# Kernel tuning notes

Hardware: AMD Instinct MI355X
Metric: run time of the kernel (lower is better)

Reference implementation:

```python
import jax, jax.numpy as jnp
from jax import lax
import numpy as np

EPS_LN = 1e-5
EPS_BN = 1e-5


def _forward(x, prior, alpha, in_proj_w, conv_w, conv_b, x_proj_weight,
             dt_projs_weight, dt_projs_bias, A_logs, Ds, out_norm_w, out_norm_b,
             out_proj_w, p2w_w1, p2w_b1, p2w_bn_w, p2w_bn_b, p2w_bn_mean,
             p2w_bn_var, p2w_w2, p2w_b2):
    Din = conv_w.shape[0]
    # in_proj (Linear2d == 1x1 conv), split into ssm branch and gate z
    xz = jnp.einsum('bchw,dc->bdhw', x, in_proj_w)          # [B, 2*Din, H, W]
    x_ssm, z = jnp.split(xz, 2, axis=1)
    # depthwise 3x3 conv + SiLU
    x_ssm = lax.conv_general_dilated(
        x_ssm, conv_w, (1, 1), 'SAME',
        dimension_numbers=('NCHW', 'OIHW', 'NCHW'),
        feature_group_count=Din) + conv_b[None, :, None, None]
    x_ssm = jax.nn.silu(x_ssm)

    B, D, H, W = x_ssm.shape
    L = H * W
    K = 4
    R = dt_projs_weight.shape[2]
    N = A_logs.shape[1]

    # cross_scan: 4 directions = row-major, col-major, and their reverses
    row = x_ssm.reshape(B, D, L)
    col = x_ssm.transpose(0, 1, 3, 2).reshape(B, D, L)
    xs = jnp.stack([row, col, row[..., ::-1], col[..., ::-1]], axis=1)  # [B,K,D,L]

    x_dbl = jnp.einsum('bkdl,kcd->bkcl', xs, x_proj_weight)  # [B,K,R+2N,L]
    dts, Bs, Cs = jnp.split(x_dbl, [R, R + N], axis=2)       # [B,K,R,L],[B,K,N,L],[B,K,N,L]
    dts = jnp.einsum('bkrl,kdr->bkdl', dts, dt_projs_weight)  # [B,K,D,L]

    A = -jnp.exp(A_logs.astype(jnp.float32)).reshape(K, D, N)
    dt = jax.nn.softplus(dts + dt_projs_bias[None, :, :, None])  # [B,K,D,L]

    dA = jnp.exp(dt[..., None] * A[None, :, :, None, :])          # [B,K,D,L,N]
    dBx = dt[..., None] * Bs.transpose(0, 1, 3, 2)[:, :, None, :, :] * xs[..., None]
    Cseq = Cs.transpose(0, 1, 3, 2)                               # [B,K,L,N]

    dA_t = jnp.moveaxis(dA, 3, 0)    # [L,B,K,D,N]
    dBx_t = jnp.moveaxis(dBx, 3, 0)  # [L,B,K,D,N]
    C_t = jnp.moveaxis(Cseq, 2, 0)   # [L,B,K,N]

    def step(h, inp):
        a, bx, c = inp
        h = h * a + bx                              # [B,K,D,N]
        y = jnp.einsum('bkdn,bkn->bkd', h, c)
        return h, y

    h0 = jnp.zeros((B, K, D, N), dtype=jnp.float32)
    _, ys = lax.scan(step, h0, (dA_t, dBx_t, C_t))  # [L,B,K,D]
    ys = jnp.moveaxis(ys, 0, 3)                     # [B,K,D,L]
    ys = ys + Ds.reshape(K, D)[None, :, :, None] * xs
    ys = ys.reshape(B, K, D, H, W)

    # prior -> per-direction guidance weights (PriorToWeights, BN in eval mode)
    g = jnp.einsum('bchw,oc->bohw', prior, p2w_w1) + p2w_b1[None, :, None, None]
    g = (g - p2w_bn_mean[None, :, None, None]) * jax.lax.rsqrt(
        p2w_bn_var[None, :, None, None] + EPS_BN)
    g = g * p2w_bn_w[None, :, None, None] + p2w_bn_b[None, :, None, None]
    g = jax.nn.relu(g)
    g = jnp.einsum('bchw,oc->bohw', g, p2w_w2) + p2w_b2[None, :, None, None]
    gw = jax.nn.sigmoid(g)                          # [B,4,H,W]
    s = jax.nn.sigmoid(alpha)                       # [1]
    Wdir = 1.0 + s * (gw - 1.0)                     # torch.lerp(ones, gw, s)
    ys = ys * Wdir[:, :, None, :, :]

    # cross_merge: inverse of cross_scan, sum of 4 directions
    ysl = ys.reshape(B, K, D, L)
    y = ysl[:, 0] + ysl[:, 2, :, ::-1]
    yt = ysl[:, 1] + ysl[:, 3, :, ::-1]
    y = y + yt.reshape(B, D, W, H).transpose(0, 1, 3, 2).reshape(B, D, L)
    y = y.reshape(B, D, H, W)

    # LayerNorm2d: normalize over channel dim
    mu = y.mean(axis=1, keepdims=True)
    var = y.var(axis=1, keepdims=True)
    y = (y - mu) * jax.lax.rsqrt(var + EPS_LN)
    y = y * out_norm_w[None, :, None, None] + out_norm_b[None, :, None, None]

    y = y * jax.nn.silu(z)
    out = jnp.einsum('bdhw,md->bmhw', y, out_proj_w)  # out_proj 1x1, no bias
    return out


def setup_inputs() -> dict:
    key = jax.random.key(0)
    ks = jax.random.split(key, 16)
    B, Dm, H, W = 8, 96, 64, 64
    Din, N, K, R, hid = 192, 1, 4, 6, 32

    def rn(k, shape, scale):
        return jax.random.normal(k, shape, jnp.float32) * scale

    return {
        'x': rn(ks[0], (B, Dm, H, W), 1.0),
        'prior': jax.random.uniform(ks[1], (B, 4, H, W), jnp.float32),
        'alpha': rn(ks[2], (1,), 1.0),
        'in_proj_w': rn(ks[3], (2 * Din, Dm), Dm ** -0.5),
        'conv_w': rn(ks[4], (Din, 1, 3, 3), 1.0 / 3.0),
        'conv_b': rn(ks[5], (Din,), 0.1),
        'x_proj_weight': rn(ks[6], (K, R + 2 * N, Din), Din ** -0.5),
        'dt_projs_weight': rn(ks[7], (K, Din, R), R ** -0.5),
        'dt_projs_bias': rn(ks[8], (K, Din), 0.5) - 4.0,
        'A_logs': jnp.tile(jnp.log(jnp.arange(1, N + 1, dtype=jnp.float32)), (K * Din, 1)),
        'Ds': jnp.ones((K * Din,), jnp.float32),
        'out_norm_w': jnp.ones((Din,), jnp.float32),
        'out_norm_b': jnp.zeros((Din,), jnp.float32),
        'out_proj_w': rn(ks[9], (Dm, Din), Din ** -0.5),
        'p2w_w1': rn(ks[10], (hid, 4), 0.5),
        'p2w_b1': jnp.zeros((hid,), jnp.float32),
        'p2w_bn_w': jnp.ones((hid,), jnp.float32),
        'p2w_bn_b': jnp.zeros((hid,), jnp.float32),
        'p2w_bn_mean': jnp.zeros((hid,), jnp.float32),
        'p2w_bn_var': jnp.ones((hid,), jnp.float32),
        'p2w_w2': rn(ks[11], (4, hid), hid ** -0.5),
        'p2w_b2': jnp.zeros((4,), jnp.float32),
    }


def reference(x, prior, alpha, in_proj_w, conv_w, conv_b, x_proj_weight,
              dt_projs_weight, dt_projs_bias, A_logs, Ds, out_norm_w, out_norm_b,
              out_proj_w, p2w_w1, p2w_b1, p2w_bn_w, p2w_bn_b, p2w_bn_mean,
              p2w_bn_var, p2w_w2, p2w_b2):
    return _forward(x, prior, alpha, in_proj_w, conv_w, conv_b, x_proj_weight,
                    dt_projs_weight, dt_projs_bias, A_logs, Ds, out_norm_w,
                    out_norm_b, out_proj_w, p2w_w1, p2w_b1, p2w_bn_w, p2w_bn_b,
                    p2w_bn_mean, p2w_bn_var, p2w_w2, p2w_b2)
```

## Files before the change

kernel.cpp:

```cpp
#include <hip/hip_runtime.h>

#define BB   8
#define CIN  96
#define DIN  192
#define HH   64
#define WW   64
#define LL   4096
#define KK   4
#define COUT 96
#define SS   128
#define LC   32

#define LOG2E 1.4426950408889634f
#define LN2   0.6931471805599453f

typedef unsigned short bf16t;
typedef float f32x2 __attribute__((ext_vector_type(2)));

__device__ __forceinline__ f32x2 pkfma(f32x2 a, f32x2 b, f32x2 c) {
#if __has_builtin(__builtin_elementwise_fma)
  return __builtin_elementwise_fma(a, b, c);
#else
  f32x2 r;
  r[0] = fmaf(a[0], b[0], c[0]);
  r[1] = fmaf(a[1], b[1], c[1]);
  return r;
#endif
}

__device__ __forceinline__ float exp2fast(float x) { return __builtin_amdgcn_exp2f(x); }
__device__ __forceinline__ float log2fast(float x) { return __builtin_amdgcn_logf(x); }
__device__ __forceinline__ float sigf(float x) { return 1.0f / (1.0f + __expf(-x)); }
__device__ __forceinline__ int trp(int p) { return ((p & 63) << 6) | (p >> 6); }
__device__ __forceinline__ int pix_of(int k, int l) {
  if (k == 0) return l;
  if (k == 1) return trp(l);
  if (k == 2) return LL - 1 - l;
  return trp(LL - 1 - l);
}
__device__ __forceinline__ float b2f(bf16t v) {
  return __uint_as_float((unsigned)v << 16);
}
__device__ __forceinline__ bf16t f2b(float f) {
  unsigned u = __float_as_uint(f);
  return (bf16t)((u + 0x7FFFu + ((u >> 16) & 1u)) >> 16);
}

__global__ __launch_bounds__(256) void gemm_in_k(const float* __restrict__ in,
                                                 const float* __restrict__ W,
                                                 bf16t* __restrict__ out) {
  const int tid = threadIdx.x;
  const int b  = blockIdx.z;
  const int o0 = blockIdx.y * 8;
  const int p0 = blockIdx.x * 1024 + tid * 4;
  const float* inb = in + (size_t)b * CIN * LL + p0;
  const float* Wb  = W + (size_t)o0 * CIN;
  f32x2 accL[8], accH[8];
#pragma unroll
  for (int j = 0; j < 8; ++j) { accL[j] = (f32x2){0.f, 0.f}; accH[j] = (f32x2){0.f, 0.f}; }
#pragma unroll 4
  for (int c = 0; c < CIN; c += 4) {
    float4 w[8];
#pragma unroll
    for (int j = 0; j < 8; ++j) w[j] = *(const float4*)&Wb[j * CIN + c];
    float4 xv[4];
#pragma unroll
    for (int t = 0; t < 4; ++t) xv[t] = *(const float4*)&inb[(size_t)(c + t) * LL];
#pragma unroll
    for (int j = 0; j < 8; ++j) {
#pragma unroll
      for (int t = 0; t < 4; ++t) {
        const float ws = t == 0 ? w[j].x : t == 1 ? w[j].y : t == 2 ? w[j].z : w[j].w;
        const f32x2 wv = {ws, ws};
        accL[j] = pkfma((f32x2){xv[t].x, xv[t].y}, wv, accL[j]);
        accH[j] = pkfma((f32x2){xv[t].z, xv[t].w}, wv, accH[j]);
      }
    }
  }
  bf16t* ob = out + (size_t)b * 384 * LL + p0;
#pragma unroll
  for (int j = 0; j < 8; ++j) {
    ushort4 st;
    st.x = f2b(accL[j][0]);
    st.y = f2b(accL[j][1]);
    st.z = f2b(accH[j][0]);
    st.w = f2b(accH[j][1]);
    *(ushort4*)&ob[(size_t)(o0 + j) * LL] = st;
  }
}

__global__ __launch_bounds__(256) void gemm_out_k(const bf16t* __restrict__ in,
                                                  const float* __restrict__ W,
                                                  float* __restrict__ out) {
  const int tid = threadIdx.x;
  const int b  = blockIdx.z;
  const int o0 = blockIdx.y * 4;
  const int p0 = blockIdx.x * 1024 + tid * 4;
  const bf16t* inb = in + (size_t)b * DIN * LL + p0;
  const float* Wb  = W + (size_t)o0 * DIN;
  f32x2 accL[4], accH[4];
#pragma unroll
  for (int j = 0; j < 4; ++j) { accL[j] = (f32x2){0.f, 0.f}; accH[j] = (f32x2){0.f, 0.f}; }
#pragma unroll 4
  for (int c = 0; c < DIN; c += 4) {
    float4 w[4];
#pragma unroll
    for (int j = 0; j < 4; ++j) w[j] = *(const float4*)&Wb[j * DIN + c];
    f32x2 xlo[4], xhi[4];
#pragma unroll
    for (int t = 0; t < 4; ++t) {
      ushort4 xu = *(const ushort4*)&inb[(size_t)(c + t) * LL];
      xlo[t] = (f32x2){b2f(xu.x), b2f(xu.y)};
      xhi[t] = (f32x2){b2f(xu.z), b2f(xu.w)};
    }
#pragma unroll
    for (int j = 0; j < 4; ++j) {
#pragma unroll
      for (int t = 0; t < 4; ++t) {
        const float ws = t == 0 ? w[j].x : t == 1 ? w[j].y : t == 2 ? w[j].z : w[j].w;
        const f32x2 wv = {ws, ws};
        accL[j] = pkfma(xlo[t], wv, accL[j]);
        accH[j] = pkfma(xhi[t], wv, accH[j]);
      }
    }
  }
  float* ob = out + (size_t)b * COUT * LL + p0;
#pragma unroll
  for (int j = 0; j < 4; ++j) {
    float4 st = make_float4(accL[j][0], accL[j][1], accH[j][0], accH[j][1]);
    *(float4*)&ob[(size_t)(o0 + j) * LL] = st;
  }
}

__global__ __launch_bounds__(256) void p2w_k(const float* __restrict__ prior,
                                             const float* __restrict__ alpha,
                                             const float* __restrict__ w1,
                                             const float* __restrict__ b1,
                                             const float* __restrict__ bnw,
                                             const float* __restrict__ bnb,
                                             const float* __restrict__ bnm,
                                             const float* __restrict__ bnv,
                                             const float* __restrict__ w2,
                                             const float* __restrict__ b2,
                                             const float* __restrict__ xpw,
                                             float* __restrict__ xpwT,
                                             float* __restrict__ Wg) {
  if (blockIdx.x == 0) {
    for (int idx = threadIdx.x; idx < KK * DIN * 8; idx += 256) {
      int kk = idx / (DIN * 8);
      int rem = idx % (DIN * 8);
      int dd = rem >> 3, c = rem & 7;
      xpwT[idx] = xpw[(kk * 8 + c) * DIN + dd];
    }
  }
  int idx = blockIdx.x * 256 + threadIdx.x;
  int p = idx & (LL - 1);
  int b = idx >> 12;
  float pr[4];
#pragma unroll
  for (int c = 0; c < 4; ++c) pr[c] = prior[((size_t)b * 4 + c) * LL + p];
  float s = sigf(alpha[0]);
  float g2[4];
#pragma unroll
  for (int j = 0; j < 4; ++j) g2[j] = b2[j];
  for (int o = 0; o < 32; ++o) {
    float g = b1[o];
#pragma unroll
    for (int c = 0; c < 4; ++c) g = fmaf(pr[c], w1[o * 4 + c], g);
    g = (g - bnm[o]) * rsqrtf(bnv[o] + 1e-5f) * bnw[o] + bnb[o];
    g = fmaxf(g, 0.0f);
#pragma unroll
    for (int j = 0; j < 4; ++j) g2[j] = fmaf(g, w2[j * 32 + o], g2[j]);
  }
#pragma unroll
  for (int j = 0; j < 4; ++j)
    Wg[((size_t)b * 4 + j) * LL + p] = 1.0f + s * (sigf(g2[j]) - 1.0f);
}

__global__ __launch_bounds__(1024) void convproj_k(const bf16t* __restrict__ xz,
                                                   const float* __restrict__ cw,
                                                   const float* __restrict__ cb,
                                                   const float* __restrict__ xpwT,
                                                   bf16t* __restrict__ xcT,
                                                   float* __restrict__ projS) {
  __shared__ float sX[96 * 65];
  __shared__ float4 sP[512];
  const int tid = threadIdx.x;
  const int b = blockIdx.y;
  const int h = blockIdx.x;
  const int px = tid & 63;
  const int ku = __builtin_amdgcn_readfirstlane((tid >> 6) & 3);
  const int hf = __builtin_amdgcn_readfirstlane((tid >> 8) & 1);
  const int q  = __builtin_amdgcn_readfirstlane(tid >> 9);
  f32x2 a01 = {0.f, 0.f}, a23 = {0.f, 0.f};

#pragma unroll
  for (int half = 0; half < 2; ++half) {
    for (int idx = tid; idx < 96 * 16; idx += 1024) {
      int ddl = idx >> 4, pq = idx & 15;
      int w0 = pq * 4;
      int dd = half * 96 + ddl;
      const bf16t* base = xz + ((size_t)b * 384 + dd) * LL + h * 64 + w0;
      const float* wp = cw + dd * 9;
      float bv = cb[dd];
      f32x2 s01 = {bv, bv}, s23 = {bv, bv};
#pragma unroll
      for (int dh = -1; dh <= 1; ++dh) {
        int hh = h + dh;
        if (hh < 0 || hh >= HH) continue;
        const bf16t* row = base + dh * 64;
        ushort4 cmu = *(const ushort4*)row;
        float cmx = b2f(cmu.x), cmy = b2f(cmu.y), cmz = b2f(cmu.z), cmw = b2f(cmu.w);
        float lf = (w0 > 0)  ? b2f(row[-1]) : 0.0f;
        float rt = (w0 < 60) ? b2f(row[4])  : 0.0f;
        float c0 = wp[(dh + 1) * 3], c1 = wp[(dh + 1) * 3 + 1], c2 = wp[(dh + 1) * 3 + 2];
        s01 = pkfma((f32x2){lf,  cmx}, (f32x2){c0, c0}, s01);
        s01 = pkfma((f32x2){cmx, cmy}, (f32x2){c1, c1}, s01);
        s01 = pkfma((f32x2){cmy, cmz}, (f32x2){c2, c2}, s01);
        s23 = pkfma((f32x2){cmy, cmz}, (f32x2){c0, c0}, s23);
        s23 = pkfma((f32x2){cmz, cmw}, (f32x2){c1, c1}, s23);
        s23 = pkfma((f32x2){cmw, rt},  (f32x2){c2, c2}, s23);
      }
      float* so = &sX[ddl * 65 + w0];
      float v0 = s01[0], v1 = s01[1], v2 = s23[0], v3 = s23[1];
      so[0] = v0 * sigf(v0);
      so[1] = v1 * sigf(v1);
      so[2] = v2 * sigf(v2);
      so[3] = v3 * sigf(v3);
    }
    __syncthreads();
    for (int idx = tid; idx < 64 * 96; idx += 1024) {
      int pp = idx / 96, ddl = idx % 96;
      xcT[((size_t)b * LL + h * 64 + pp) * DIN + half * 96 + ddl] =
          f2b(sX[ddl * 65 + pp]);
    }
    {
      const int ddl0 = q * 48;
      const float* wp = xpwT + (size_t)ku * (DIN * 8) + (half * 96 + ddl0) * 8 + hf * 4;
#pragma unroll 8
      for (int d48 = 0; d48 < 48; ++d48) {
        float xv = sX[(ddl0 + d48) * 65 + px];
        const float4 w4 = *(const float4*)(wp + d48 * 8);
        const f32x2 xv2 = {xv, xv};
        a01 = pkfma(xv2, (f32x2){w4.x, w4.y}, a01);
        a23 = pkfma(xv2, (f32x2){w4.z, w4.w}, a23);
      }
    }
    __syncthreads();
  }
  const int slot = tid & 511;
  if (q == 1) sP[slot] = make_float4(a01[0], a01[1], a23[0], a23[1]);
  __syncthreads();
  if (q == 0) {
    float4 o = sP[slot];
    float r0 = a01[0] + o.x, r1 = a01[1] + o.y, r2 = a23[0] + o.z, r3 = a23[1] + o.w;
    const int p = h * 64 + px;
    int l;
    if (ku == 0) l = p;
    else if (ku == 1) l = trp(p);
    else if (ku == 2) l = LL - 1 - p;
    else l = LL - 1 - trp(p);
    float* pb = projS + (((size_t)b * KK + ku) * LL + l) * 8 + hf * 4;
    *(float4*)pb = make_float4(r0, r1, r2, r3);
  }
}

__global__ __launch_bounds__(192) void scan_part_k(const bf16t* __restrict__ xcT,
                                                   const float* __restrict__ projS,
                                                   const float* __restrict__ dtw,
                                                   const float* __restrict__ dtb,
                                                   const float* __restrict__ A_logs,
                                                   float* __restrict__ carrP,
                                                   float* __restrict__ carrH) {
  const int s = blockIdx.x, kp = blockIdx.y, b = blockIdx.z;
  const int d = threadIdx.x;
  const int kA = kp, kB = kp + 2;
  const int s2 = SS - 1 - s;
  const int kdA = kA * DIN + d, kdB = kB * DIN + d;
  float wrA[6], wrB[6];
#pragma unroll
  for (int r = 0; r < 6; ++r) { wrA[r] = dtw[kdA * 6 + r]; wrB[r] = dtw[kdB * 6 + r]; }
  const float biasA = dtb[kdA], biasB = dtb[kdB];
  const float AaA = -__expf(A_logs[kdA]), AaB = -__expf(A_logs[kdB]);
  const int l0 = s * LC;
  const int p0 = pix_of(kA, l0);
  const int dp = pix_of(kA, l0 + 1) - p0;
  const bf16t* xp = xcT + ((size_t)b * LL + p0) * DIN + d;
  const long xstep = (long)dp * DIN;
  const float* prA = projS + (((size_t)b * KK + kA) * LL + l0) * 8;
  const float* prB = projS + (((size_t)b * KK + kB) * LL + s2 * LC + (LC - 1)) * 8;
  float PA = 1.0f, HA = 0.0f, PB = 1.0f, HB = 0.0f;
#pragma unroll 2
  for (int j = 0; j < LC; ++j) {
    float4 a0 = *(const float4*)prA;
    float4 a1 = *(const float4*)(prA + 4);
    prA += 8;
    float4 b0 = *(const float4*)prB;
    float4 b1 = *(const float4*)(prB + 4);
    prB -= 8;
    float xv = b2f(*xp);
    xp += xstep;
    {
      float dtr = biasA;
      dtr = fmaf(a0.x, wrA[0], dtr);
      dtr = fmaf(a0.y, wrA[1], dtr);
      dtr = fmaf(a0.z, wrA[2], dtr);
      dtr = fmaf(a0.w, wrA[3], dtr);
      dtr = fmaf(a1.x, wrA[4], dtr);
      dtr = fmaf(a1.y, wrA[5], dtr);
      float e = exp2fast(fminf(dtr, 80.0f) * LOG2E);
      float u = log2fast(1.0f + e);
      float a = exp2fast(u * AaA);
      float dt = u * LN2;
      HA = fmaf(a, HA, dt * a1.z * xv);
      PA *= a;
    }
    {
      float dtr = biasB;
      dtr = fmaf(b0.x, wrB[0], dtr);
      dtr = fmaf(b0.y, wrB[1], dtr);
      dtr = fmaf(b0.z, wrB[2], dtr);
      dtr = fmaf(b0.w, wrB[3], dtr);
      dtr = fmaf(b1.x, wrB[4], dtr);
      dtr = fmaf(b1.y, wrB[5], dtr);
      float e = exp2fast(fminf(dtr, 80.0f) * LOG2E);
      float u = log2fast(1.0f + e);
      float a = exp2fast(u * AaB);
      float dt = u * LN2;
      HB = fmaf(PB, dt * b1.z * xv, HB);
      PB *= a;
    }
  }
  size_t oA = ((size_t)((b * KK + kA) * SS + s)) * DIN + d;
  size_t oB = ((size_t)((b * KK + kB) * SS + s2)) * DIN + d;
  carrP[oA] = PA;
  carrH[oA] = HA;
  carrP[oB] = PB;
  carrH[oB] = HB;
}

__global__ __launch_bounds__(192) void scan_fix_k(const float* __restrict__ carrP,
                                                  const float* __restrict__ carrH,
                                                  float* __restrict__ h0) {
  const int k = blockIdx.x, b = blockIdx.y, d = threadIdx.x;
  size_t base = ((size_t)(b * KK + k)) * SS * DIN + d;
  float h = 0.0f;
#pragma unroll 4
  for (int s = 0; s < SS; ++s) {
    h0[base + (size_t)s * DIN] = h;
    h = fmaf(carrP[base + (size_t)s * DIN], h, carrH[base + (size_t)s * DIN]);
  }
}

__global__ __launch_bounds__(192) void scan_apply_k(const bf16t* __restrict__ xcT,
                                                    const float* __restrict__ projS,
                                                    const float* __restrict__ Wg,
                                                    const float* __restrict__ h0,
                                                    const float* __restrict__ dtw,
                                                    const float* __restrict__ dtb,
                                                    const float* __restrict__ A_logs,
                                                    const float* __restrict__ Ds,
                                                    bf16t* __restrict__ ymT,
                                                    bf16t* __restrict__ ymT2) {
  const int s = blockIdx.x, kp = blockIdx.y, b = blockIdx.z;
  const int d = threadIdx.x;
  __shared__ float sAcc[LC * DIN];
  float xr[LC];
  {
    const int k = kp, kd = k * DIN + d;
    float wr[6];
#pragma unroll
    for (int r = 0; r < 6; ++r) wr[r] = dtw[kd * 6 + r];
    const float bias = dtb[kd];
    const float Aa = -__expf(A_logs[kd]);
    const float Dv = Ds[kd];
    const int l0 = s * LC;
    const int p0 = pix_of(k, l0);
    const int dp = pix_of(k, l0 + 1) - p0;
    const bf16t* xp = xcT + ((size_t)b * LL + p0) * DIN + d;
    const long xstep = (long)dp * DIN;
    const float* pr = projS + (((size_t)b * KK + k) * LL + l0) * 8;
    const float* wg = Wg + ((size_t)b * KK + k) * LL + l0;
    float h = h0[((size_t)((b * KK + k) * SS + s)) * DIN + d];
#pragma unroll
    for (int j = 0; j < LC; ++j) {
      float4 q0 = *(const float4*)pr;
      float4 q1 = *(const float4*)(pr + 4);
      pr += 8;
      float xv = b2f(*xp);
      xp += xstep;
      xr[j] = xv;
      float dtr = bias;
      dtr = fmaf(q0.x, wr[0], dtr);
      dtr = fmaf(q0.y, wr[1], dtr);
      dtr = fmaf(q0.z, wr[2], dtr);
      dtr = fmaf(q0.w, wr[3], dtr);
      dtr = fmaf(q1.x, wr[4], dtr);
      dtr = fmaf(q1.y, wr[5], dtr);
      float e = exp2fast(fminf(dtr, 80.0f) * LOG2E);
      float u = log2fast(1.0f + e);
      float a = exp2fast(u * Aa);
      float dt = u * LN2;
      h = fmaf(a, h, dt * q1.z * xv);
      sAcc[j * DIN + d] = fmaf(h, q1.w, Dv * xv) * wg[j];
    }
  }
  {
    const int k = kp + 2, kd = k * DIN + d;
    const int s2 = SS - 1 - s;
    float wr[6];
#pragma unroll
    for (int r = 0; r < 6; ++r) wr[r] = dtw[kd * 6 + r];
    const float bias = dtb[kd];
    const float Aa = -__expf(A_logs[kd]);
    const float Dv = Ds[kd];
    const int l0 = s2 * LC;
    const float* pr = projS + (((size_t)b * KK + k) * LL + l0) * 8;
    const float* wg = Wg + ((size_t)b * KK + k) * LL + l0;
    float h = h0[((size_t)((b * KK + k) * SS + s2)) * DIN + d];
#pragma unroll
    for (int j = 0; j < LC; ++j) {
      float4 q0 = *(const float4*)pr;
      float4 q1 = *(const float4*)(pr + 4);
      pr += 8;
      float xv = xr[LC - 1 - j];
      float dtr = bias;
      dtr = fmaf(q0.x, wr[0], dtr);
      dtr = fmaf(q0.y, wr[1], dtr);
      dtr = fmaf(q0.z, wr[2], dtr);
      dtr = fmaf(q0.w, wr[3], dtr);
      dtr = fmaf(q1.x, wr[4], dtr);
      dtr = fmaf(q1.y, wr[5], dtr);
      float e = exp2fast(fminf(dtr, 80.0f) * LOG2E);
      float u = log2fast(1.0f + e);
      float a = exp2fast(u * Aa);
      float dt = u * LN2;
      h = fmaf(a, h, dt * q1.z * xv);
      float y = fmaf(h, q1.w, Dv * xv) * wg[j];
      sAcc[(LC - 1 - j) * DIN + d] += y;
    }
  }
  bf16t* dst;
  if (kp == 0)
    dst = ymT + (size_t)b * (384 * (size_t)LL) + (size_t)(s * LC) * DIN + d;
  else
    dst = ymT2 + ((size_t)b * LL + s * LC) * DIN + d;
#pragma unroll 4
  for (int j = 0; j < LC; ++j) dst[(size_t)j * DIN] = f2b(sAcc[j * DIN + d]);
}

__global__ __launch_bounds__(256) void ln_silu_k(const bf16t* __restrict__ ymT,
                                                 const bf16t* __restrict__ ymT2,
                                                 const bf16t* __restrict__ xz,
                                                 const float* __restrict__ gamma,
                                                 const float* __restrict__ beta,
                                                 bf16t* __restrict__ u) {
  const int b = blockIdx.y;
  const int h = blockIdx.x;
  const int p0 = h * 64;
  __shared__ float sY[64 * 193];
  __shared__ float sS[4][64], sQ[4][64];
  const int tid = threadIdx.x;
  const bf16t* ymb = ymT + (size_t)b * (384 * (size_t)LL);
  for (int idx = tid; idx < 64 * DIN; idx += 256) {
    int pp = idx / DIN, dd = idx % DIN;
    float v = b2f(ymb[(size_t)(p0 + pp) * DIN + dd]) +
              b2f(ymT2[((size_t)b * LL + pp * 64 + h) * DIN + dd]);
    sY[pp * 193 + dd] = v;
  }
  __syncthreads();
  const int px = tid & 63, g = tid >> 6;
  float sum = 0.0f, ss = 0.0f;
  for (int dd = g * 48; dd < g * 48 + 48; ++dd) {
    float v = sY[px * 193 + dd];
    sum += v;
    ss = fmaf(v, v, ss);
  }
  sS[g][px] = sum;
  sQ[g][px] = ss;
  __syncthreads();
  sum = sS[0][px] + sS[1][px] + sS[2][px] + sS[3][px];
  ss  = sQ[0][px] + sQ[1][px] + sQ[2][px] + sQ[3][px];
  const float mu = sum * (1.0f / DIN);
  float var = ss * (1.0f / DIN) - mu * mu;
  const float rstd = rsqrtf(fmaxf(var, 0.0f) + 1e-5f);
  const bf16t* zb = xz + ((size_t)b * 384 + DIN) * LL + p0 + px;
  bf16t* ub = u + (size_t)b * DIN * LL + p0 + px;
  for (int dd = g * 48; dd < g * 48 + 48; ++dd) {
    float v = sY[px * 193 + dd];
    float z = b2f(zb[(size_t)dd * LL]);
    float tn = fmaf((v - mu) * rstd, gamma[dd], beta[dd]);
    ub[(size_t)dd * LL] = f2b(tn * (z * sigf(z)));
  }
}

extern "C" void kernel_launch(void* const* d_in, const int* in_sizes, int n_in,
                              void* d_out, int out_size, void* d_ws, size_t ws_size,
                              hipStream_t stream) {
  const float* x      = (const float*)d_in[0];
  const float* prior  = (const float*)d_in[1];
  const float* alpha  = (const float*)d_in[2];
  const float* ipw    = (const float*)d_in[3];
  const float* cw     = (const float*)d_in[4];
  const float* cb     = (const float*)d_in[5];
  const float* xpw    = (const float*)d_in[6];
  const float* dtw    = (const float*)d_in[7];
  const float* dtb    = (const float*)d_in[8];
  const float* A_logs = (const float*)d_in[9];
  const float* Ds     = (const float*)d_in[10];
  const float* onw    = (const float*)d_in[11];
  const float* onb    = (const float*)d_in[12];
  const float* opw    = (const float*)d_in[13];
  const float* w1     = (const float*)d_in[14];
  const float* b1     = (const float*)d_in[15];
  const float* bnw    = (const float*)d_in[16];
  const float* bnb    = (const float*)d_in[17];
  const float* bnm    = (const float*)d_in[18];
  const float* bnv    = (const float*)d_in[19];
  const float* w2     = (const float*)d_in[20];
  const float* b2     = (const float*)d_in[21];
  float* out = (float*)d_out;

  char* ws = (char*)d_ws;
  bf16t* xz    = (bf16t*)(ws);
  bf16t* xcT   = (bf16t*)(ws + 25165824);
  bf16t* ymT2  = (bf16t*)(ws + 37748736);
  float* projS = (float*)(ws + 50331648);
  float* Wgb   = (float*)(ws + 54525952);
  float* carrP = (float*)(ws + 55050240);
  float* carrH = (float*)(ws + 58195968);
  float* h0b   = (float*)(ws + 61341696);
  float* xpwT  = (float*)(ws + 64487424);
  bf16t* ymT   = xz;
  bf16t* u     = xcT;

  gemm_in_k<<<dim3(LL / 1024, 384 / 8, BB), 256, 0, stream>>>(x, ipw, xz);
  p2w_k<<<(BB * LL) / 256, 256, 0, stream>>>(prior, alpha, w1, b1, bnw, bnb, bnm,
                                             bnv, w2, b2, xpw, xpwT, Wgb);
  convproj_k<<<dim3(HH, BB), 1024, 0, stream>>>(xz, cw, cb, xpwT, xcT, projS);
  scan_part_k<<<dim3(SS, 2, BB), 192, 0, stream>>>(xcT, projS, dtw, dtb, A_logs,
                                                   carrP, carrH);
  scan_fix_k<<<dim3(KK, BB), 192, 0, stream>>>(carrP, carrH, h0b);
  scan_apply_k<<<dim3(SS, 2, BB), 192, 0, stream>>>(xcT, projS, Wgb, h0b, dtw, dtb,
                                                    A_logs, Ds, ymT, ymT2);
  ln_silu_k<<<dim3(HH, BB), 256, 0, stream>>>(ymT, ymT2, xz, onw, onb, u);
  gemm_out_k<<<dim3(LL / 1024, COUT / 4, BB), 256, 0, stream>>>(u, opw, out);
}
```

Baseline: 181.1 us.

## Use bf16 MFMA for the input projection GEMM

Replaces the scalar packed-FMA input projection with a matrix-core kernel. Each block stages a 32-pixel tile of x as bf16 in LDS and multiplies it by all 384 output rows using 16x16x32 bf16 MFMA, with one wave handling 96 rows. The weights are pre-converted to bf16 inside the p2w kernel, which now has to run before the GEMM. Inputs are rounded to bf16 before the multiply, which lowers accuracy. The output stores are narrow 2-byte writes spread across rows, which may coalesce poorly.

```diff
diff --git a/kernel.cpp b/kernel.cpp
--- a/kernel.cpp
+++ b/kernel.cpp
@@ -16,6 +16,8 @@
 
 typedef unsigned short bf16t;
 typedef float f32x2 __attribute__((ext_vector_type(2)));
+typedef float f32x4 __attribute__((ext_vector_type(4)));
+typedef short bf16x8s __attribute__((ext_vector_type(8)));
 
 __device__ __forceinline__ f32x2 pkfma(f32x2 a, f32x2 b, f32x2 c) {
 #if __has_builtin(__builtin_elementwise_fma)
@@ -46,46 +48,46 @@
   return (bf16t)((u + 0x7FFFu + ((u >> 16) & 1u)) >> 16);
 }
 
-__global__ __launch_bounds__(256) void gemm_in_k(const float* __restrict__ in,
-                                                 const float* __restrict__ W,
-                                                 bf16t* __restrict__ out) {
+__global__ __launch_bounds__(256) void gemm_in_mfma_k(const float* __restrict__ x,
+                                                      const bf16t* __restrict__ Wb,
+                                                      bf16t* __restrict__ out) {
+  __shared__ bf16t ldsB[32 * 104];
   const int tid = threadIdx.x;
-  const int b  = blockIdx.z;
-  const int o0 = blockIdx.y * 8;
-  const int p0 = blockIdx.x * 1024 + tid * 4;
-  const float* inb = in + (size_t)b * CIN * LL + p0;
-  const float* Wb  = W + (size_t)o0 * CIN;
-  f32x2 accL[8], accH[8];
-#pragma unroll
-  for (int j = 0; j < 8; ++j) { accL[j] = (f32x2){0.f, 0.f}; accH[j] = (f32x2){0.f, 0.f}; }
-#pragma unroll 4
-  for (int c = 0; c < CIN; c += 4) {
-    float4 w[8];
-#pragma unroll
-    for (int j = 0; j < 8; ++j) w[j] = *(const float4*)&Wb[j * CIN + c];
-    float4 xv[4];
-#pragma unroll
-    for (int t = 0; t < 4; ++t) xv[t] = *(const float4*)&inb[(size_t)(c + t) * LL];
-#pragma unroll
-    for (int j = 0; j < 8; ++j) {
-#pragma unroll
-      for (int t = 0; t < 4; ++t) {
-        const float ws = t == 0 ? w[j].x : t == 1 ? w[j].y : t == 2 ? w[j].z : w[j].w;
-        const f32x2 wv = {ws, ws};
-        accL[j] = pkfma((f32x2){xv[t].x, xv[t].y}, wv, accL[j]);
-        accH[j] = pkfma((f32x2){xv[t].z, xv[t].w}, wv, accH[j]);
-      }
-    }
-  }
+  const int b = blockIdx.z;
+  const int p0 = blockIdx.x * 32;
+  for (int idx = tid; idx < CIN * 32; idx += 256) {
+    int c = idx >> 5, px = idx & 31;
+    ldsB[px * 104 + c] = f2b(x[((size_t)b * CIN + c) * LL + p0 + px]);
+  }
+  __syncthreads();
+  const int wave = tid >> 6, lane = tid & 63;
+  const int lm = lane & 15, kc = lane >> 4;
+  bf16x8s bfrag[2][3];
+#pragma unroll
+  for (int nf = 0; nf < 2; ++nf)
+#pragma unroll
+    for (int ks = 0; ks < 3; ++ks)
+      bfrag[nf][ks] = *(const bf16x8s*)&ldsB[(nf * 16 + lm) * 104 + ks * 32 + kc * 8];
   bf16t* ob = out + (size_t)b * 384 * LL + p0;
 #pragma unroll
-  for (int j = 0; j < 8; ++j) {
-    ushort4 st;
-    st.x = f2b(accL[j][0]);
-    st.y = f2b(accL[j][1]);
-    st.z = f2b(accH[j][0]);
-    st.w = f2b(accH[j][1]);
-    *(ushort4*)&ob[(size_t)(o0 + j) * LL] = st;
+  for (int mti = 0; mti < 6; ++mti) {
+    const int o0 = (wave * 6 + mti) * 16;
+    bf16x8s afrag[3];
+#pragma unroll
+    for (int ks = 0; ks < 3; ++ks)
+      afrag[ks] = *(const bf16x8s*)&Wb[(size_t)(o0 + lm) * CIN + ks * 32 + kc * 8];
+    f32x4 acc0 = {0.f, 0.f, 0.f, 0.f};
+    f32x4 acc1 = {0.f, 0.f, 0.f, 0.f};
+#pragma unroll
+    for (int ks = 0; ks < 3; ++ks) {
+      acc0 = __builtin_amdgcn_mfma_f32_16x16x32_bf16(afrag[ks], bfrag[0][ks], acc0, 0, 0, 0);
+      acc1 = __builtin_amdgcn_mfma_f32_16x16x32_bf16(afrag[ks], bfrag[1][ks], acc1, 0, 0, 0);
+    }
+#pragma unroll
+    for (int r = 0; r < 4; ++r) {
+      ob[(size_t)(o0 + kc * 4 + r) * LL + lm]      = f2b(acc0[r]);
+      ob[(size_t)(o0 + kc * 4 + r) * LL + 16 + lm] = f2b(acc1[r]);
+    }
   }
 }
 
@@ -143,7 +145,9 @@
                                              const float* __restrict__ w2,
                                              const float* __restrict__ b2,
                                              const float* __restrict__ xpw,
+                                             const float* __restrict__ ipw,
                                              float* __restrict__ xpwT,
+                                             bf16t* __restrict__ ipwb,
                                              float* __restrict__ Wg) {
   if (blockIdx.x == 0) {
     for (int idx = threadIdx.x; idx < KK * DIN * 8; idx += 256) {
@@ -152,6 +156,10 @@
       int dd = rem >> 3, c = rem & 7;
       xpwT[idx] = xpw[(kk * 8 + c) * DIN + dd];
     }
+  }
+  if (blockIdx.x == 1) {
+    for (int idx = threadIdx.x; idx < 384 * CIN; idx += 256)
+      ipwb[idx] = f2b(ipw[idx]);
   }
   int idx = blockIdx.x * 256 + threadIdx.x;
   int p = idx & (LL - 1);
@@ -531,12 +539,13 @@
   float* carrH = (float*)(ws + 58195968);
   float* h0b   = (float*)(ws + 61341696);
   float* xpwT  = (float*)(ws + 64487424);
+  bf16t* ipwb  = (bf16t*)(ws + 64512000);
   bf16t* ymT   = xz;
   bf16t* u     = xcT;
 
-  gemm_in_k<<<dim3(LL / 1024, 384 / 8, BB), 256, 0, stream>>>(x, ipw, xz);
   p2w_k<<<(BB * LL) / 256, 256, 0, stream>>>(prior, alpha, w1, b1, bnw, bnb, bnm,
-                                             bnv, w2, b2, xpw, xpwT, Wgb);
+                                             bnv, w2, b2, xpw, ipw, xpwT, ipwb, Wgb);
+  gemm_in_mfma_k<<<dim3(LL / 32, 1, BB), 256, 0, stream>>>(x, ipwb, xz);
   convproj_k<<<dim3(HH, BB), 1024, 0, stream>>>(xz, cw, cb, xpwT, xcT, projS);
   scan_part_k<<<dim3(SS, 2, BB), 192, 0, stream>>>(xcT, projS, dtw, dtb, A_logs,
                                                    carrP, carrH);
```

After: 174.6 us. 1.04x faster.
